# Performance work log

Hardware: AMD Instinct MI355X
Metric: run time of the kernel (lower is better)

Reference implementation:

```python
import jax, jax.numpy as jnp
import numpy as np

EPS_BN = 1e-5
DIVERSITY_TEMP = 100.0  # lucidrains codebook_diversity_temperature default
COMMIT_W = 1.0
DIVERSITY_W = 1.0
ORTHO_W = 1.0


def conv1d(x, w, b=None, stride=1, pad=0):
    # x: [B,C,T], w: [O,I,K] (torch layout)
    y = jax.lax.conv_general_dilated(x, w, (stride,), [(pad, pad)],
                                     dimension_numbers=('NCH', 'OIH', 'NCH'))
    if b is not None:
        y = y + b[None, :, None]
    return y


def conv1d_transpose(x, w_torch, stride, pad):
    # torch ConvTranspose1d weight: (in, out, k). Equivalent input-dilated conv
    # with flipped kernel and padding k-1-pad.
    w = jnp.flip(jnp.transpose(w_torch, (1, 0, 2)), axis=2)  # -> (out,in,k)
    k = w.shape[2]
    p = k - 1 - pad
    return jax.lax.conv_general_dilated(x, w, (1,), [(p, p)],
                                        lhs_dilation=(stride,),
                                        dimension_numbers=('NCH', 'OIH', 'NCH'))


def batchnorm(x, g, b):
    # training-mode BatchNorm1d: stats over (batch, time) per channel
    m = x.mean(axis=(0, 2), keepdims=True)
    v = x.var(axis=(0, 2), keepdims=True)
    return (x - m) * jax.lax.rsqrt(v + EPS_BN) * g[None, :, None] + b[None, :, None]


def setup_inputs():
    key = jax.random.key(0)
    ks = jax.random.split(key, 10)
    f32 = jnp.float32
    rn = lambda k, shape, s: jax.random.normal(k, shape, f32) * s
    return {
        'x': jax.random.normal(ks[0], (8, 1, 24000), f32),
        # encoder: 1->16->32->64
        'w1': rn(ks[1], (16, 1, 5), 0.3), 'b1': jnp.zeros(16, f32),
        'g1': jnp.ones(16, f32), 'be1': jnp.zeros(16, f32),
        'w2': rn(ks[2], (32, 16, 5), 0.1), 'b2': jnp.zeros(32, f32),
        'g2': jnp.ones(32, f32), 'be2': jnp.zeros(32, f32),
        'w3': rn(ks[3], (64, 32, 25), 0.05), 'b3': jnp.zeros(64, f32),
        'g3': jnp.ones(64, f32), 'be3': jnp.zeros(64, f32),
        # VQ codebook [codebook_size=8192, dim=64]
        'embed': jax.random.normal(ks[4], (8192, 64), f32),
        # decoder
        'dw1': rn(ks[5], (64, 64, 25), 0.05),  # ConvTranspose1d weight (in,out,k)
        'dg1': jnp.ones(64, f32), 'dbe1': jnp.zeros(64, f32),
        'dw2': rn(ks[6], (64, 64, 5), 0.1), 'db2': jnp.zeros(64, f32),
        'dg2': jnp.ones(64, f32), 'dbe2': jnp.zeros(64, f32),
        'dw3': rn(ks[7], (1, 64, 1), 0.2), 'db3': jnp.zeros(1, f32),
        # fixed random subset for orthogonal reg (orthogonal_reg_max_codes=256)
        'ortho_idx': jax.random.randint(ks[8], (256,), 0, 8192),
    }


def reference(x, w1, b1, g1, be1, w2, b2, g2, be2, w3, b3, g3, be3,
              embed, dw1, dg1, dbe1, dw2, db2, dg2, dbe2, dw3, db3, ortho_idx):
    # ---- encoder ----
    h = batchnorm(jax.nn.silu(conv1d(x, w1, b1, 1, 2)), g1, be1)
    h = batchnorm(jax.nn.silu(conv1d(h, w2, b2, 1, 2)), g2, be2)
    z = batchnorm(jnp.tanh(conv1d(h, w3, b3, 12, 12)), g3, be3)  # [B,64,N]
    B, C, N = z.shape
    zf = jnp.transpose(z, (0, 2, 1)).reshape(B * N, C)  # [B*N, 64]

    # ---- VQ: nearest neighbor over codebook ----
    d2 = (jnp.sum(zf * zf, -1, keepdims=True) - 2.0 * (zf @ embed.T)
          + jnp.sum(embed * embed, -1)[None, :])          # [B*N, K]
    dist = jnp.sqrt(jnp.clip(d2, 1e-12))                  # euclidean (cdist p=2)
    idx = jnp.argmin(d2, axis=-1)                         # [B*N]
    q = embed[idx]                                        # codebook gather

    commit = jnp.mean((jax.lax.stop_gradient(q) - zf) ** 2)

    prob = jax.nn.softmax(-dist * DIVERSITY_TEMP, axis=-1)
    avg_prob = prob.mean(axis=0)                          # [K]
    diversity = jnp.sum(avg_prob * jnp.log(jnp.clip(avg_prob, 1e-30)))

    codes = embed[ortho_idx]                              # [256, 64]
    normed = codes * jax.lax.rsqrt(jnp.sum(codes * codes, -1, keepdims=True) + 1e-12)
    cos = normed @ normed.T
    n = codes.shape[0]
    ortho = jnp.sum(cos * cos) / (n * n) - 1.0 / n

    loss = COMMIT_W * commit + DIVERSITY_W * diversity + ORTHO_W * ortho

    # straight-through estimator
    q_st = zf + jax.lax.stop_gradient(q - zf)
    zq = jnp.transpose(q_st.reshape(B, N, C), (0, 2, 1))  # [B,64,N]

    # ---- decoder ----
    d = batchnorm(jax.nn.silu(conv1d_transpose(zq, dw1, 12, 12)), dg1, dbe1)
    d = batchnorm(jax.nn.silu(conv1d(d, dw2, db2, 1, 2)), dg2, dbe2)
    recon = conv1d(d, dw3, db3, 1, 0)

    T = x.shape[2]
    cur = recon.shape[2]
    if cur > T:
        recon = recon[:, :, :T]
    elif cur < T:
        recon = jnp.pad(recon, ((0, 0), (0, 0), (0, T - cur)))
    return recon, idx.reshape(B, N), loss, (commit, diversity, ortho)
```

## Files before the change

kernel.cpp:

```cpp
#include <hip/hip_runtime.h>
#include <math.h>
#include <float.h>

#define DEV __device__ __forceinline__

#define BB 8
#define TT 24000
#define TD 23989
#define NZ 2000
#define ROWS 16000
#define NE 8192
#define NCG 8

typedef __attribute__((ext_vector_type(8))) short bf16x8;
typedef __attribute__((ext_vector_type(4))) float f32x4;

__device__ double g_st[640];
__device__ double g_misc[2];
__device__ float  g_e2[NE];
__device__ float  g_avg[NE];
__device__ float  g_z2[ROWS];
__device__ float  g_rdm[ROWS];
__device__ int    g_rix[ROWS];
__device__ float  g_ob[256 * 64];
__device__ float  g_pmd[ROWS * NCG];
__device__ int    g_pmi[ROWS * NCG];
__device__ int    g_pcc[ROWS * NCG];
__device__ float2 g_cand[ROWS * 256];
__device__ unsigned short g_zbh[ROWS * 64], g_zbl[ROWS * 64];
__device__ unsigned short g_ebh[NE * 64],  g_ebl[NE * 64];
__device__ float  g_s1[16], g_sh1[16];
__device__ float  g_s2[32], g_sh2[32];
__device__ float  g_sd1[64], g_shd1[64];
__device__ float  g_w2f[2560];
__device__ float  g_b2f[32];
__device__ float  g_w3f[64 * 32 * 25];
__device__ float  g_b3f[64];
__device__ float  g_dw2f[64 * 5 * 64];
__device__ float  g_db2f[64];
__device__ float  g_dw1t[64 * 64 * 25];
__device__ float  g_zbn[ROWS * 64];
__device__ double g_zbnd[ROWS * 64];
__device__ float  g_zq[BB * 64 * NZ];
__device__ float  g_y1[BB * 16 * TT];
__device__ float  g_zpre[BB * 64 * NZ];
__device__ float  g_yd1[BB * 64 * TD];
__device__ float  g_y2[BB * 32 * TT];
__device__ float  g_yd2[BB * 64 * TD];

DEV float wsum(float v){
  #pragma unroll
  for (int o = 32; o; o >>= 1) v += __shfl_xor(v, o, 64);
  return v;
}
DEV int clampc(int c){ return c < 0 ? 0 : (c > NE - 1 ? NE - 1 : c); }
DEV float bss(unsigned short s){ union { unsigned u; float f; } v; v.u = ((unsigned)s) << 16; return v.f; }
DEV unsigned short f2bs(float f){
  union { float f; unsigned u; } v; v.f = f;
  unsigned r = (v.u + 0x7FFF + ((v.u >> 16) & 1)) >> 16;
  return (unsigned short)r;
}

__global__ void k_zero(){
  int i = blockIdx.x * 256 + threadIdx.x;
  if (i < 640) g_st[i] = 0.0;
  if (i < 2) g_misc[i] = 0.0;
  if (i < NE) g_avg[i] = 0.f;
}

__global__ void k_embprep(const float* __restrict__ embed){
  int gt = blockIdx.x * 256 + threadIdx.x;
  int gs = gridDim.x * 256;
  for (int i = gt; i < NE * 64; i += gs){
    float v = embed[i];
    unsigned short h = f2bs(v);
    g_ebh[i] = h;
    g_ebl[i] = f2bs(v - bss(h));
  }
  for (int c = gt; c < NE; c += gs){
    float s = 0.f;
    for (int j = 0; j < 64; j++){ float v = embed[c * 64 + j]; s += v * v; }
    g_e2[c] = s;
  }
}

__global__ void k_zsplit(){
  int i = blockIdx.x * 256 + threadIdx.x;
  if (i < ROWS * 64){
    float v = g_zbn[i];
    unsigned short h = f2bs(v);
    g_zbh[i] = h;
    g_zbl[i] = f2bs(v - bss(h));
  }
}

__global__ void k_conv1(const float* __restrict__ x, const float* __restrict__ w1,
                        const float* __restrict__ b1){
  int b = blockIdx.y, t0 = blockIdx.x * 256, tid = threadIdx.x;
  __shared__ float xs[260], wl[80], bl[16], sacc[16], qacc[16];
  if (tid < 80) wl[tid] = w1[tid];
  if (tid < 16){ bl[tid] = b1[tid]; sacc[tid] = 0.f; qacc[tid] = 0.f; }
  for (int i = tid; i < 260; i += 256){ int g = t0 - 2 + i; xs[i] = ((unsigned)g < TT) ? x[b * TT + g] : 0.f; }
  __syncthreads();
  int t = t0 + tid;
  bool ok = t < TT;
  float xv[5];
  #pragma unroll
  for (int k = 0; k < 5; k++) xv[k] = xs[tid + k];
  float out[16];
  #pragma unroll
  for (int c = 0; c < 16; c++){
    float a = bl[c];
    #pragma unroll
    for (int k = 0; k < 5; k++) a += wl[c * 5 + k] * xv[k];
    float o = ok ? a / (1.f + expf(-a)) : 0.f;
    out[c] = o;
    if (ok) g_y1[(b * 16 + c) * TT + t] = o;
  }
  int lane = tid & 63;
  #pragma unroll
  for (int c = 0; c < 16; c++){
    float s = wsum(out[c]);
    float q = wsum(out[c] * out[c]);
    if (lane == 0){ atomicAdd(&sacc[c], s); atomicAdd(&qacc[c], q); }
  }
  __syncthreads();
  if (tid < 16){ atomicAdd(&g_st[tid * 2], (double)sacc[tid]); atomicAdd(&g_st[tid * 2 + 1], (double)qacc[tid]); }
}

__global__ void k_fold2(const float* __restrict__ g1, const float* __restrict__ be1,
                        const float* __restrict__ w2, const float* __restrict__ b2){
  int tid = threadIdx.x;
  if (blockIdx.x == 0 && tid < 16){
    double m = g_st[tid * 2] / 192000.0, v = g_st[tid * 2 + 1] / 192000.0 - m * m;
    float s = g1[tid] / sqrtf((float)v + 1e-5f);
    g_s1[tid] = s; g_sh1[tid] = be1[tid] - (float)m * s;
  }
  if (blockIdx.x == 0 && tid < 32) g_b2f[tid] = b2[tid];
  int gt = blockIdx.x * 256 + tid;
  for (int i = gt; i < 2560; i += 8 * 256){
    int co = i & 31, r = i >> 5, k = r % 5, ci = r / 5;
    g_w2f[i] = w2[(co * 16 + ci) * 5 + k];
  }
}

__global__ void __launch_bounds__(256) k_conv2(){
  int b = blockIdx.y, t0 = blockIdx.x * 256, tid = threadIdx.x;
  __shared__ float xs[16][260];
  __shared__ float sacc[32], qacc[32];
  __shared__ float s1l[16], sh1l[16];
  int lane = tid & 63, wv = tid >> 6;
  int cb = wv * 8;
  if (tid < 32){ sacc[tid] = 0.f; qacc[tid] = 0.f; }
  if (tid < 16){ s1l[tid] = g_s1[tid]; sh1l[tid] = g_sh1[tid]; }
  __syncthreads();
  for (int i = tid; i < 16 * 260; i += 256){
    int ci = i / 260, tt = i - ci * 260, g = t0 - 2 + tt;
    xs[ci][tt] = ((unsigned)g < TT) ? (s1l[ci] * g_y1[(b * 16 + ci) * TT + g] + sh1l[ci]) : 0.f;
  }
  __syncthreads();
  float acc[4][8];
  #pragma unroll
  for (int j = 0; j < 4; j++)
    #pragma unroll
    for (int i = 0; i < 8; i++) acc[j][i] = g_b2f[cb + i];
  for (int ci = 0; ci < 16; ci++){
    #pragma unroll
    for (int k = 0; k < 5; k++){
      const float4* wp = (const float4*)(g_w2f + (ci * 5 + k) * 32 + cb);
      float4 w0 = wp[0], w1v = wp[1];
      float wr[8] = { w0.x, w0.y, w0.z, w0.w, w1v.x, w1v.y, w1v.z, w1v.w };
      #pragma unroll
      for (int j = 0; j < 4; j++){
        float xv = xs[ci][lane + 64 * j + k];
        #pragma unroll
        for (int i = 0; i < 8; i++) acc[j][i] += wr[i] * xv;
      }
    }
  }
  #pragma unroll
  for (int i = 0; i < 8; i++){
    int co = cb + i;
    float s = 0.f, q = 0.f;
    #pragma unroll
    for (int j = 0; j < 4; j++){
      int t = t0 + lane + 64 * j;
      bool ok = t < TT;
      float a = acc[j][i];
      float o = ok ? a / (1.f + expf(-a)) : 0.f;
      if (ok) g_y2[(b * 32 + co) * TT + t] = o;
      s += o; q += o * o;
    }
    s = wsum(s); q = wsum(q);
    if (lane == 0){ atomicAdd(&sacc[co], s); atomicAdd(&qacc[co], q); }
  }
  __syncthreads();
  if (tid < 32){ atomicAdd(&g_st[128 + tid * 2], (double)sacc[tid]); atomicAdd(&g_st[128 + tid * 2 + 1], (double)qacc[tid]); }
}

__global__ void k_fold3(const float* __restrict__ g2, const float* __restrict__ be2,
                        const float* __restrict__ w3, const float* __restrict__ b3){
  int tid = threadIdx.x;
  if (blockIdx.x == 0 && tid < 32){
    double m = g_st[128 + tid * 2] / 192000.0, v = g_st[128 + tid * 2 + 1] / 192000.0 - m * m;
    float s = g2[tid] / sqrtf((float)v + 1e-5f);
    g_s2[tid] = s; g_sh2[tid] = be2[tid] - (float)m * s;
  }
  if (blockIdx.x == 0 && tid >= 64 && tid < 128) g_b3f[tid - 64] = b3[tid - 64];
  int gt = blockIdx.x * 256 + tid;
  for (int i = gt; i < 64 * 32 * 25; i += 64 * 256){
    int co = i & 63, r = i >> 6, k = r % 25, ci = r / 25;
    g_w3f[i] = w3[(co * 32 + ci) * 25 + k];
  }
}

__global__ void __launch_bounds__(256) k_conv3(){
  __shared__ float xs[32][400];
  __shared__ float s2l[32], sh2l[32];
  int tid = threadIdx.x, b = blockIdx.y, t0 = blockIdx.x * 32;
  int lane = tid & 63, wv = tid >> 6;
  int cb = wv * 16;
  int tl = lane & 31, h = lane >> 5;
  if (tid < 32){ s2l[tid] = g_s2[tid]; sh2l[tid] = g_sh2[tid]; }
  __syncthreads();
  int p0 = t0 * 12 - 12;
  for (int i = tid; i < 32 * 397; i += 256){
    int ci = i / 397, pp = i - ci * 397, g = p0 + pp;
    xs[ci][pp] = ((unsigned)g < TT) ? (s2l[ci] * g_y2[(b * 32 + ci) * TT + g] + sh2l[ci]) : 0.f;
  }
  __syncthreads();
  float acc[16];
  #pragma unroll
  for (int i = 0; i < 16; i++) acc[i] = 0.f;
  for (int cii = 0; cii < 16; cii++){
    int ci = h * 16 + cii;
    #pragma unroll
    for (int k = 0; k < 25; k++){
      float xv = xs[ci][tl * 12 + k];
      const float4* wp = (const float4*)(g_w3f + (ci * 25 + k) * 64 + cb);
      float4 a0 = wp[0], a1 = wp[1], a2 = wp[2], a3 = wp[3];
      acc[0] += a0.x * xv; acc[1] += a0.y * xv; acc[2] += a0.z * xv; acc[3] += a0.w * xv;
      acc[4] += a1.x * xv; acc[5] += a1.y * xv; acc[6] += a1.z * xv; acc[7] += a1.w * xv;
      acc[8] += a2.x * xv; acc[9] += a2.y * xv; acc[10] += a2.z * xv; acc[11] += a2.w * xv;
      acc[12] += a3.x * xv; acc[13] += a3.y * xv; acc[14] += a3.z * xv; acc[15] += a3.w * xv;
    }
  }
  #pragma unroll
  for (int i = 0; i < 16; i++) acc[i] += __shfl_xor(acc[i], 32, 64);
  int t = t0 + tl;
  if (h == 0 && t < NZ){
    #pragma unroll
    for (int i = 0; i < 16; i++)
      g_zpre[(b * 64 + cb + i) * NZ + t] = tanhf(acc[i] + g_b3f[cb + i]);
  }
}

__global__ void k_stats(int which, int L, int stoff){
  const float* p = (which == 0) ? g_zpre : (which == 1) ? g_yd1 : g_yd2;
  int co = blockIdx.y, t0 = blockIdx.x * 256, tid = threadIdx.x;
  int t = t0 + tid;
  float s = 0.f, q = 0.f;
  if (t < L){
    for (int b = 0; b < BB; b++){ float v = p[(b * 64 + co) * L + t]; s += v; q += v * v; }
  }
  s = wsum(s); q = wsum(q);
  __shared__ float sa[4], qa[4];
  int w = tid >> 6, lane = tid & 63;
  if (lane == 0){ sa[w] = s; qa[w] = q; }
  __syncthreads();
  if (tid == 0){
    atomicAdd(&g_st[stoff + co * 2], (double)(sa[0] + sa[1] + sa[2] + sa[3]));
    atomicAdd(&g_st[stoff + co * 2 + 1], (double)(qa[0] + qa[1] + qa[2] + qa[3]));
  }
}

__global__ void k_zbn(const float* __restrict__ g3, const float* __restrict__ be3){
  __shared__ float tile[64][65];
  __shared__ float s3[64], sh3[64];
  __shared__ double s3d[64], sh3d[64];
  int tid = threadIdx.x, b = blockIdx.y, n0 = blockIdx.x * 64;
  if (tid < 64){
    double m = g_st[256 + tid * 2] / 16000.0, v = g_st[256 + tid * 2 + 1] / 16000.0 - m * m;
    double sd = (double)g3[tid] / sqrt(v + 1e-5);
    double shd = (double)be3[tid] - m * sd;
    s3d[tid] = sd; sh3d[tid] = shd;
    s3[tid] = (float)sd; sh3[tid] = (float)shd;
  }
  __syncthreads();
  for (int i = tid; i < 64 * 64; i += 256){
    int c = i >> 6, nn = i & 63, n = n0 + nn;
    tile[c][nn] = (n < NZ) ? (s3[c] * g_zpre[(b * 64 + c) * NZ + n] + sh3[c]) : 0.f;
  }
  __syncthreads();
  int lane = tid & 63;
  for (int it = 0; it < 16; ++it){
    int nn = (tid >> 6) + it * 4;
    int n = n0 + nn, c = lane;
    if (n < NZ){
      float v = tile[c][nn];
      int row = b * NZ + n;
      g_zbn[row * 64 + c] = v;
      g_zbnd[row * 64 + c] = s3d[c] * (double)g_zpre[(b * 64 + c) * NZ + n] + sh3d[c];
      float s = wsum(v * v);
      if (lane == 0) g_z2[row] = s;
    }
  }
}

__global__ void __launch_bounds__(256) k_vq1(){
  __shared__ unsigned short bsh[64 * 72];
  __shared__ unsigned short bsl[64 * 72];
  __shared__ float2 ring[64][16];
  __shared__ int cnt[64];
  int tid = threadIdx.x, lane = tid & 63, w = tid >> 6;
  int q = lane >> 4, col = lane & 15;
  int rowbase = blockIdx.x * 64 + w * 16;
  int cbase = blockIdx.y * 1024;
  int grp = blockIdx.y;
  if (tid < 64) cnt[tid] = 0;
  #pragma unroll
  for (int i = 0; i < 4; i++)
    ring[w * 16 + (lane & 15)][(lane >> 4) * 4 + i] = make_float2(FLT_MAX, __int_as_float(NE - 1));
  bf16x8 ah0, ah1, al0, al1;
  {
    const unsigned short* zh = g_zbh + (rowbase + col) * 64;
    const unsigned short* zl = g_zbl + (rowbase + col) * 64;
    ah0 = *(const bf16x8*)(zh + q * 8);
    ah1 = *(const bf16x8*)(zh + 32 + q * 8);
    al0 = *(const bf16x8*)(zl + q * 8);
    al1 = *(const bf16x8*)(zl + 32 + q * 8);
  }
  float z2r[4];
  #pragma unroll
  for (int r = 0; r < 4; r++) z2r[r] = g_z2[rowbase + q * 4 + r];
  float thr[4], lmin[4]; int lamc[4];
  #pragma unroll
  for (int r = 0; r < 4; r++){ thr[r] = FLT_MAX; lmin[r] = FLT_MAX; lamc[r] = NE - 1; }
  float runmin[4] = {FLT_MAX, FLT_MAX, FLT_MAX, FLT_MAX};
  for (int ch = 0; ch < 16; ++ch){
    __syncthreads();
    {
      int cl = tid >> 2, seg = tid & 3;
      int cglob = cbase + ch * 64 + cl;
      *(int4*)&bsh[cl * 72 + seg * 16]     = *(const int4*)(g_ebh + cglob * 64 + seg * 16);
      *(int4*)&bsh[cl * 72 + seg * 16 + 8] = *(const int4*)(g_ebh + cglob * 64 + seg * 16 + 8);
      *(int4*)&bsl[cl * 72 + seg * 16]     = *(const int4*)(g_ebl + cglob * 64 + seg * 16);
      *(int4*)&bsl[cl * 72 + seg * 16 + 8] = *(const int4*)(g_ebl + cglob * 64 + seg * 16 + 8);
    }
    __syncthreads();
    float d2s[4][4];
    float tmin[4] = {FLT_MAX, FLT_MAX, FLT_MAX, FLT_MAX};
    #pragma unroll
    for (int t = 0; t < 4; t++){
      int ct = cbase + ch * 64 + t * 16;
      const unsigned short* bhp = &bsh[(t * 16 + col) * 72];
      const unsigned short* blp = &bsl[(t * 16 + col) * 72];
      bf16x8 bh0 = *(const bf16x8*)(bhp + q * 8);
      bf16x8 bh1 = *(const bf16x8*)(bhp + 32 + q * 8);
      bf16x8 bl0 = *(const bf16x8*)(blp + q * 8);
      bf16x8 bl1 = *(const bf16x8*)(blp + 32 + q * 8);
      f32x4 acc = {0.f, 0.f, 0.f, 0.f};
      acc = __builtin_amdgcn_mfma_f32_16x16x32_bf16(al0, bh0, acc, 0, 0, 0);
      acc = __builtin_amdgcn_mfma_f32_16x16x32_bf16(al1, bh1, acc, 0, 0, 0);
      acc = __builtin_amdgcn_mfma_f32_16x16x32_bf16(ah0, bl0, acc, 0, 0, 0);
      acc = __builtin_amdgcn_mfma_f32_16x16x32_bf16(ah1, bl1, acc, 0, 0, 0);
      acc = __builtin_amdgcn_mfma_f32_16x16x32_bf16(ah0, bh0, acc, 0, 0, 0);
      acc = __builtin_amdgcn_mfma_f32_16x16x32_bf16(ah1, bh1, acc, 0, 0, 0);
      float e2c = g_e2[ct + col];
      #pragma unroll
      for (int r = 0; r < 4; r++){
        float d = z2r[r] + e2c - 2.f * acc[r];
        d2s[t][r] = d;
        if (d < lmin[r]){ lmin[r] = d; lamc[r] = ct + col; }
        tmin[r] = fminf(tmin[r], d);
      }
    }
    #pragma unroll
    for (int r = 0; r < 4; r++){
      float m = tmin[r];
      m = fminf(m, __shfl_xor(m, 1, 64));
      m = fminf(m, __shfl_xor(m, 2, 64));
      m = fminf(m, __shfl_xor(m, 4, 64));
      m = fminf(m, __shfl_xor(m, 8, 64));
      if (m < runmin[r]){
        runmin[r] = m;
        thr[r] = m + 0.71f * sqrtf(fmaxf(m, 0.f)) + 0.13f;
      }
    }
    #pragma unroll
    for (int t = 0; t < 4; t++){
      int ct = cbase + ch * 64 + t * 16;
      bool any = false;
      #pragma unroll
      for (int r = 0; r < 4; r++) if (d2s[t][r] < thr[r]) any = true;
      if (__ballot(any)){
        #pragma unroll
        for (int r = 0; r < 4; r++){
          if (d2s[t][r] < thr[r]){
            int lr = w * 16 + q * 4 + r;
            int s = atomicAdd(&cnt[lr], 1) & 15;
            ring[lr][s] = make_float2(sqrtf(fmaxf(d2s[t][r], 1e-12f)), __int_as_float(ct + col));
          }
        }
      }
    }
  }
  __syncthreads();
  #pragma unroll
  for (int r = 0; r < 4; r++){
    float m = lmin[r]; int c = lamc[r];
    #pragma unroll
    for (int o = 1; o <= 8; o <<= 1){
      float om = __shfl_xor(m, o, 64);
      int oc = __shfl_xor(c, o, 64);
      if (om < m || (om == m && oc < c)){ m = om; c = oc; }
    }
    if (col == 0){
      int gr = rowbase + q * 4 + r;
      g_pmd[gr * NCG + grp] = m;
      g_pmi[gr * NCG + grp] = c;
    }
  }
  if (lane < 16){
    int lr = w * 16 + lane;
    g_pcc[(rowbase + lane) * NCG + grp] = cnt[lr];
  }
  #pragma unroll
  for (int i = 0; i < 4; i++){
    int idx = lane * 4 + i;
    int lr = idx >> 4, s = idx & 15;
    g_cand[(rowbase + lr) * 256 + grp * 16 + s] = ring[w * 16 + lr][s];
  }
}

__global__ void k_vq1b(){
  int row = blockIdx.x * 256 + threadIdx.x;
  if (row >= ROWS) return;
  float best = FLT_MAX; int bi = NE - 1;
  for (int cg = 0; cg < NCG; ++cg){
    float d = g_pmd[row * NCG + cg]; int i = g_pmi[row * NCG + cg];
    if (d < best || (d == best && i < bi)){ best = d; bi = i; }
  }
  g_rdm[row] = sqrtf(fmaxf(best, 1e-12f));
  g_rix[row] = bi;
}

__global__ void __launch_bounds__(256) k_vq3(const float* __restrict__ embed,
                                             float* __restrict__ outIdx){
  __shared__ int   ccode[4][144];
  __shared__ float cdst[4][144];
  __shared__ int   cn[4];
  __shared__ double bsum[4];
  int w = threadIdx.x >> 6, lane = threadIdx.x & 63;
  int row = blockIdx.x * 4 + w;
  float dmin = g_rdm[row];
  int seedc = clampc(g_rix[row]);
  if (lane == 0){ cn[w] = 0; ccode[w][0] = seedc; }
  __syncthreads();
  if (lane == 0) cn[w] = 1;
  int grp = lane & 7;
  int sub = lane >> 3;
  int cnt = g_pcc[row * NCG + grp]; if (cnt > 16) cnt = 16;
  int s0 = sub * 2, s1 = s0 + 2; if (s1 > cnt) s1 = cnt;
  for (int s = s0; s < s1; ++s){
    float2 cd = g_cand[row * 256 + grp * 16 + s];
    float dist = cd.x; int c = clampc(__float_as_int(cd.y));
    if (dist <= dmin + 0.353f && c != seedc){
      int i = atomicAdd(&cn[w], 1);
      ccode[w][i] = c;
    }
  }
  __syncthreads();
  int n = cn[w];
  double zdl = g_zbnd[row * 64 + lane];
  double bd = DBL_MAX; int bc = NE - 1;
  for (int i = 0; i < n; i++){
    int c = ccode[w][i];
    double diff = zdl - (double)embed[c * 64 + lane];
    double d = diff * diff;
    #pragma unroll
    for (int o = 32; o; o >>= 1) d += __shfl_xor(d, o, 64);
    if (lane == 0) cdst[w][i] = (float)d;
    if (d < bd || (d == bd && c < bc)){ bd = d; bc = c; }
  }
  __syncthreads();
  float dminE = (float)sqrt(bd);
  float Zp = 0.f;
  for (int i = lane; i < n; i += 64)
    Zp += expf(-100.f * (sqrtf(cdst[w][i]) - dminE));
  float Z = fmaxf(wsum(Zp), 1e-30f);
  if (lane == 0){
    g_rix[row] = bc;
    outIdx[row] = (float)bc;
    bsum[w] = bd;
  }
  for (int i = lane; i < n; i += 64)
    atomicAdd(&g_avg[ccode[w][i]], expf(-100.f * (sqrtf(cdst[w][i]) - dminE)) / Z);
  __syncthreads();
  if (threadIdx.x == 0)
    atomicAdd(&g_misc[0], bsum[0] + bsum[1] + bsum[2] + bsum[3]);
}

__global__ void k_orthoprep(const float* __restrict__ embed, const int* __restrict__ oidx){
  int tid = threadIdx.x;
  int c = clampc(oidx[tid]);
  float s = 0.f;
  for (int j = 0; j < 64; j++){ float v = embed[c * 64 + j]; s += v * v; }
  float r = 1.f / sqrtf(s + 1e-12f);
  for (int j = 0; j < 64; j++) g_ob[tid * 64 + j] = embed[c * 64 + j] * r;
}

__global__ void k_ortho(){
  int w = threadIdx.x >> 6, lane = threadIdx.x & 63;
  int i = blockIdx.x * 4 + w;
  float acc = 0.f;
  for (int j = lane; j < 256; j += 64){
    float d = 0.f;
    for (int k = 0; k < 64; k++) d += g_ob[i * 64 + k] * g_ob[j * 64 + k];
    acc += d * d;
  }
  acc = wsum(acc);
  if (lane == 0) atomicAdd(&g_misc[1], (double)acc);
}

__global__ void k_div(float* __restrict__ outS){
  int tid = threadIdx.x;
  double part = 0.0;
  for (int c = tid; c < NE; c += 256){
    double p = (double)g_avg[c] / 16000.0;
    double pc = p < 1e-30 ? 1e-30 : p;
    part += p * log(pc);
  }
  __shared__ double red[256];
  red[tid] = part; __syncthreads();
  for (int o = 128; o; o >>= 1){ if (tid < o) red[tid] += red[tid + o]; __syncthreads(); }
  if (tid == 0){
    double diversity = red[0];
    double commit = g_misc[0] / (double)(ROWS * 64);
    double ortho = g_misc[1] / 65536.0 - 1.0 / 256.0;
    double loss = commit + diversity + ortho;
    outS[0] = (float)loss;
    outS[1] = (float)commit;
    outS[2] = (float)diversity;
    outS[3] = (float)ortho;
  }
}

__global__ void k_zq(const float* __restrict__ embed){
  __shared__ float tile[64][65];
  int tid = threadIdx.x, b = blockIdx.y, n0 = blockIdx.x * 64;
  for (int i = tid; i < 64 * 64; i += 256){
    int nn = i >> 6, c = i & 63;
    int n = n0 + nn;
    int code = (n < NZ) ? clampc(g_rix[b * NZ + n]) : 0;
    tile[c][nn] = embed[code * 64 + c];
  }
  __syncthreads();
  for (int i = tid; i < 64 * 64; i += 256){
    int c = i >> 6, nn = i & 63;
    int n = n0 + nn;
    if (n < NZ) g_zq[(b * 64 + c) * NZ + n] = tile[c][nn];
  }
}

__global__ void k_folddw1(const float* __restrict__ dw1){
  int gt = blockIdx.x * 256 + threadIdx.x;
  for (int i = gt; i < 64 * 64 * 25; i += 100 * 256){
    int co = i & 63, r = i >> 6, k = r % 25, ci = r / 25;
    g_dw1t[i] = dw1[(ci * 64 + co) * 25 + (24 - k)];
  }
}

__global__ void __launch_bounds__(256, 3) k_dconv1(){
  __shared__ float xsd[16][260];
  __shared__ float wsh[4][64][28];
  __shared__ float sacc[4], qacc[4];
  int tid = threadIdx.x, b = blockIdx.y;
  int cb = blockIdx.z * 4;
  int t0 = blockIdx.x * 3072;
  int nb = blockIdx.x * 256 - 1;
  int w = tid >> 6, lane = tid & 63;
  if (tid < 4){ sacc[tid] = 0.f; qacc[tid] = 0.f; }
  for (int i = tid; i < 6400; i += 256){
    int c = i & 3, r = i >> 2;
    int k = r % 25, ci = r / 25;
    wsh[c][ci][k] = g_dw1t[r * 64 + cb + c];
  }
  float acc[4][12];
  #pragma unroll
  for (int q = 0; q < 4; q++)
    #pragma unroll
    for (int p = 0; p < 12; p++) acc[q][p] = 0.f;
  for (int cc = 0; cc < 4; ++cc){
    __syncthreads();
    for (int i = tid; i < 16 * 259; i += 256){
      int ci = i / 259, nl = i - ci * 259;
      int n = nb + nl;
      xsd[ci][nl] = ((unsigned)n < NZ) ? g_zq[(b * 64 + cc * 16 + ci) * NZ + n] : 0.f;
    }
    __syncthreads();
    #pragma unroll 2
    for (int ci = 0; ci < 16; ++ci){
      int cia = cc * 16 + ci;
      const float4* xp = (const float4*)&xsd[ci][4 * lane];
      float4 xA = xp[0], xB = xp[1];
      float xv[6] = { xA.x, xA.y, xA.z, xA.w, xB.x, xB.y };
      const float4* wp = (const float4*)&wsh[w][cia][0];
      float4 w0 = wp[0], w1 = wp[1], w2 = wp[2], w3 = wp[3], w4 = wp[4], w5 = wp[5];
      float wv[25] = { w0.x, w0.y, w0.z, w0.w, w1.x, w1.y, w1.z, w1.w,
                       w2.x, w2.y, w2.z, w2.w, w3.x, w3.y, w3.z, w3.w,
                       w4.x, w4.y, w4.z, w4.w, w5.x, w5.y, w5.z, w5.w,
                       wsh[w][cia][24] };
      #pragma unroll
      for (int q = 0; q < 4; ++q){
        acc[q][0] += wv[0] * xv[q];
        acc[q][0] += wv[12] * xv[q + 1];
        acc[q][0] += wv[24] * xv[q + 2];
        #pragma unroll
        for (int p = 1; p < 12; ++p){
          acc[q][p] += wv[12 - p] * xv[q + 1];
          acc[q][p] += wv[24 - p] * xv[q + 2];
        }
      }
    }
  }
  bool full = (t0 + 3072 <= TD);
  float s = 0.f, qs = 0.f;
  float* dst = &g_yd1[(b * 64 + cb + w) * TD + t0 + lane * 48];
  #pragma unroll
  for (int q = 0; q < 4; ++q){
    float o[12];
    #pragma unroll
    for (int p = 0; p < 12; ++p){
      int t = t0 + lane * 48 + q * 12 + p;
      float a = acc[q][p];
      float v = (t < TD) ? a / (1.f + expf(-a)) : 0.f;
      o[p] = v; s += v; qs += v * v;
    }
    if (full){
      ((float4*)(dst + q * 12))[0] = make_float4(o[0], o[1], o[2], o[3]);
      ((float4*)(dst + q * 12))[1] = make_float4(o[4], o[5], o[6], o[7]);
      ((float4*)(dst + q * 12))[2] = make_float4(o[8], o[9], o[10], o[11]);
    } else {
      #pragma unroll
      for (int p = 0; p < 12; ++p){
        int t = t0 + lane * 48 + q * 12 + p;
        if (t < TD) dst[q * 12 + p] = o[p];
      }
    }
  }
  s = wsum(s); qs = wsum(qs);
  if (lane == 0){ atomicAdd(&sacc[w], s); atomicAdd(&qacc[w], qs); }
  __syncthreads();
  if (tid < 4){
    atomicAdd(&g_st[384 + (cb + tid) * 2], (double)sacc[tid]);
    atomicAdd(&g_st[384 + (cb + tid) * 2 + 1], (double)qacc[tid]);
  }
}

__global__ void k_foldd2(const float* __restrict__ dg1, const float* __restrict__ dbe1,
                         const float* __restrict__ dw2, const float* __restrict__ db2){
  int tid = threadIdx.x;
  if (blockIdx.x == 0 && tid < 64){
    double m = g_st[384 + tid * 2] / 191912.0, v = g_st[384 + tid * 2 + 1] / 191912.0 - m * m;
    float sc = dg1[tid] / sqrtf((float)v + 1e-5f);
    g_sd1[tid] = sc; g_shd1[tid] = dbe1[tid] - (float)m * sc;
    g_db2f[tid] = db2[tid];
  }
  int gt = blockIdx.x * 256 + tid;
  for (int i = gt; i < 64 * 5 * 64; i += 32 * 256){
    int co = i & 63, r = i >> 6, k = r % 5, ci = r / 5;
    g_dw2f[i] = dw2[(co * 64 + ci) * 5 + k];
  }
}

__global__ void __launch_bounds__(256) k_dconv2(){
  __shared__ float xs[32][132];
  __shared__ float sdl[64], shdl[64];
  __shared__ float sacc[64], qacc[64];
  int tid = threadIdx.x, b = blockIdx.y, t0 = blockIdx.x * 128;
  int lane = tid & 63, wv = tid >> 6;
  int cb = wv * 16;
  if (tid < 64){ sdl[tid] = g_sd1[tid]; shdl[tid] = g_shd1[tid]; sacc[tid] = 0.f; qacc[tid] = 0.f; }
  float acc[2][16];
  #pragma unroll
  for (int j = 0; j < 2; j++)
    #pragma unroll
    for (int i = 0; i < 16; i++) acc[j][i] = g_db2f[cb + i];
  for (int half = 0; half < 2; ++half){
    __syncthreads();
    for (int i = tid; i < 32 * 132; i += 256){
      int ci = i / 132, tt = i - ci * 132, g = t0 - 2 + tt;
      int cia = half * 32 + ci;
      xs[ci][tt] = ((unsigned)g < TD) ? (sdl[cia] * g_yd1[(b * 64 + cia) * TD + g] + shdl[cia]) : 0.f;
    }
    __syncthreads();
    for (int ci = 0; ci < 32; ci++){
      int cia = half * 32 + ci;
      #pragma unroll
      for (int k = 0; k < 5; k++){
        const float4* wp = (const float4*)(g_dw2f + (cia * 5 + k) * 64 + cb);
        float4 w0 = wp[0], w1 = wp[1], w2v = wp[2], w3v = wp[3];
        float wr[16] = { w0.x, w0.y, w0.z, w0.w, w1.x, w1.y, w1.z, w1.w,
                         w2v.x, w2v.y, w2v.z, w2v.w, w3v.x, w3v.y, w3v.z, w3v.w };
        #pragma unroll
        for (int j = 0; j < 2; j++){
          float xv = xs[ci][lane + 64 * j + k];
          #pragma unroll
          for (int i = 0; i < 16; i++) acc[j][i] += wr[i] * xv;
        }
      }
    }
  }
  #pragma unroll
  for (int i = 0; i < 16; i++){
    int co = cb + i;
    float s = 0.f, q = 0.f;
    #pragma unroll
    for (int j = 0; j < 2; j++){
      int t = t0 + lane + 64 * j;
      bool ok = t < TD;
      float a = acc[j][i];
      float o = ok ? a / (1.f + expf(-a)) : 0.f;
      if (ok) g_yd2[(b * 64 + co) * TD + t] = o;
      s += o; q += o * o;
    }
    s = wsum(s); q = wsum(q);
    if (lane == 0){ atomicAdd(&sacc[co], s); atomicAdd(&qacc[co], q); }
  }
  __syncthreads();
  if (tid < 64){
    atomicAdd(&g_st[512 + tid * 2], (double)sacc[tid]);
    atomicAdd(&g_st[512 + tid * 2 + 1], (double)qacc[tid]);
  }
}

__global__ void k_recon(const float* __restrict__ dg2, const float* __restrict__ dbe2,
                        const float* __restrict__ dw3, const float* __restrict__ db3,
                        float* __restrict__ outR){
  __shared__ float wf[64];
  __shared__ float bsh2;
  int tid = threadIdx.x, b = blockIdx.y, t0 = blockIdx.x * 256;
  if (tid < 64){
    double m = g_st[512 + tid * 2] / 191912.0, v = g_st[512 + tid * 2 + 1] / 191912.0 - m * m;
    float sc = dg2[tid] / sqrtf((float)v + 1e-5f);
    float shv = dbe2[tid] - (float)m * sc;
    wf[tid] = dw3[tid] * sc;
    float contrib = wsum(dw3[tid] * shv);
    if (tid == 0) bsh2 = db3[0] + contrib;
  }
  __syncthreads();
  int t = t0 + tid;
  if (t < TT){
    if (t < TD){
      float a = bsh2;
      for (int ci = 0; ci < 64; ci++) a += wf[ci] * g_yd2[(b * 64 + ci) * TD + t];
      outR[b * TT + t] = a;
    } else {
      outR[b * TT + t] = 0.f;
    }
  }
}

extern "C" void kernel_launch(void* const* d_in, const int* in_sizes, int n_in,
                              void* d_out, int out_size, void* d_ws, size_t ws_size,
                              hipStream_t stream){
  (void)in_sizes; (void)n_in; (void)out_size; (void)d_ws; (void)ws_size;
  const float* x    = (const float*)d_in[0];
  const float* w1   = (const float*)d_in[1];
  const float* b1   = (const float*)d_in[2];
  const float* g1   = (const float*)d_in[3];
  const float* be1  = (const float*)d_in[4];
  const float* w2   = (const float*)d_in[5];
  const float* b2   = (const float*)d_in[6];
  const float* g2   = (const float*)d_in[7];
  const float* be2  = (const float*)d_in[8];
  const float* w3   = (const float*)d_in[9];
  const float* b3   = (const float*)d_in[10];
  const float* g3   = (const float*)d_in[11];
  const float* be3  = (const float*)d_in[12];
  const float* embed= (const float*)d_in[13];
  const float* dw1  = (const float*)d_in[14];
  const float* dg1  = (const float*)d_in[15];
  const float* dbe1 = (const float*)d_in[16];
  const float* dw2  = (const float*)d_in[17];
  const float* db2  = (const float*)d_in[18];
  const float* dg2  = (const float*)d_in[19];
  const float* dbe2 = (const float*)d_in[20];
  const float* dw3  = (const float*)d_in[21];
  const float* db3  = (const float*)d_in[22];
  const int* oidx   = (const int*)d_in[23];

  float* out    = (float*)d_out;
  float* outIdx = out + 192000;
  float* outS   = out + 208000;

  hipLaunchKernelGGL(k_zero, dim3(32), dim3(256), 0, stream);
  hipLaunchKernelGGL(k_embprep, dim3(64), dim3(256), 0, stream, embed);
  hipLaunchKernelGGL(k_conv1, dim3(94, 8), dim3(256), 0, stream, x, w1, b1);
  hipLaunchKernelGGL(k_fold2, dim3(8), dim3(256), 0, stream, g1, be1, w2, b2);
  hipLaunchKernelGGL(k_conv2, dim3(94, 8), dim3(256), 0, stream);
  hipLaunchKernelGGL(k_fold3, dim3(64), dim3(256), 0, stream, g2, be2, w3, b3);
  hipLaunchKernelGGL(k_conv3, dim3(63, 8), dim3(256), 0, stream);
  hipLaunchKernelGGL(k_stats, dim3(8, 64), dim3(256), 0, stream, 0, NZ, 256);
  hipLaunchKernelGGL(k_zbn, dim3(32, 8), dim3(256), 0, stream, g3, be3);
  hipLaunchKernelGGL(k_zsplit, dim3(4000), dim3(256), 0, stream);
  hipLaunchKernelGGL(k_vq1, dim3(250, 8), dim3(256), 0, stream);
  hipLaunchKernelGGL(k_vq1b, dim3(63), dim3(256), 0, stream);
  hipLaunchKernelGGL(k_vq3, dim3(4000), dim3(256), 0, stream, embed, outIdx);
  hipLaunchKernelGGL(k_orthoprep, dim3(1), dim3(256), 0, stream, embed, oidx);
  hipLaunchKernelGGL(k_ortho, dim3(64), dim3(256), 0, stream);
  hipLaunchKernelGGL(k_div, dim3(1), dim3(256), 0, stream, outS);
  hipLaunchKernelGGL(k_zq, dim3(32, 8), dim3(256), 0, stream, embed);
  hipLaunchKernelGGL(k_folddw1, dim3(100), dim3(256), 0, stream, dw1);
  hipLaunchKernelGGL(k_dconv1, dim3(8, 8, 16), dim3(256), 0, stream);
  hipLaunchKernelGGL(k_foldd2, dim3(32), dim3(256), 0, stream, dg1, dbe1, dw2, db2);
  hipLaunchKernelGGL(k_dconv2, dim3(188, 8), dim3(256), 0, stream);
  hipLaunchKernelGGL(k_recon, dim3(94, 8), dim3(256), 0, stream, dg2, dbe2, dw3, db3, out);
}
```

Baseline: 963.4 us.

## Retile decoder conv2 with register blocking, shared-memory weights and vector stores

```diff
diff --git a/kernel.cpp b/kernel.cpp
--- a/kernel.cpp
+++ b/kernel.cpp
@@ -674,64 +674,94 @@
   }
 }
 
-__global__ void __launch_bounds__(256) k_dconv2(){
-  __shared__ float xs[32][132];
+__global__ void __launch_bounds__(256, 2) k_dconv2(){
+  __shared__ float xs[16][772];
+  __shared__ float wch[16 * 5 * 32];
   __shared__ float sdl[64], shdl[64];
-  __shared__ float sacc[64], qacc[64];
-  int tid = threadIdx.x, b = blockIdx.y, t0 = blockIdx.x * 128;
+  __shared__ float sacc[32], qacc[32];
+  int tid = threadIdx.x, b = blockIdx.y, bz = blockIdx.z;
+  int t0 = blockIdx.x * 768;
   int lane = tid & 63, wv = tid >> 6;
-  int cb = wv * 16;
-  if (tid < 64){ sdl[tid] = g_sd1[tid]; shdl[tid] = g_shd1[tid]; sacc[tid] = 0.f; qacc[tid] = 0.f; }
-  float acc[2][16];
-  #pragma unroll
-  for (int j = 0; j < 2; j++)
-    #pragma unroll
-    for (int i = 0; i < 16; i++) acc[j][i] = g_db2f[cb + i];
-  for (int half = 0; half < 2; ++half){
+  int cb = bz * 32 + wv * 8;
+  if (tid < 64){ sdl[tid] = g_sd1[tid]; shdl[tid] = g_shd1[tid]; }
+  if (tid < 32){ sacc[tid] = 0.f; qacc[tid] = 0.f; }
+  float acc[12][8];
+  #pragma unroll
+  for (int j = 0; j < 12; j++)
+    #pragma unroll
+    for (int i = 0; i < 8; i++) acc[j][i] = g_db2f[cb + i];
+  for (int ch = 0; ch < 4; ++ch){
     __syncthreads();
-    for (int i = tid; i < 32 * 132; i += 256){
-      int ci = i / 132, tt = i - ci * 132, g = t0 - 2 + tt;
-      int cia = half * 32 + ci;
+    for (int i = tid; i < 16 * 772; i += 256){
+      int ci = i / 772, tt = i - ci * 772, g = t0 - 2 + tt;
+      int cia = ch * 16 + ci;
       xs[ci][tt] = ((unsigned)g < TD) ? (sdl[cia] * g_yd1[(b * 64 + cia) * TD + g] + shdl[cia]) : 0.f;
     }
+    for (int i = tid; i < 2560; i += 256){
+      int r = i >> 5, c = i & 31;
+      wch[i] = g_dw2f[(ch * 80 + r) * 64 + bz * 32 + c];
+    }
     __syncthreads();
-    for (int ci = 0; ci < 32; ci++){
-      int cia = half * 32 + ci;
+    for (int ci = 0; ci < 16; ++ci){
+      float xv[3][8];
       #pragma unroll
-      for (int k = 0; k < 5; k++){
-        const float4* wp = (const float4*)(g_dw2f + (cia * 5 + k) * 64 + cb);
-        float4 w0 = wp[0], w1 = wp[1], w2v = wp[2], w3v = wp[3];
-        float wr[16] = { w0.x, w0.y, w0.z, w0.w, w1.x, w1.y, w1.z, w1.w,
-                         w2v.x, w2v.y, w2v.z, w2v.w, w3v.x, w3v.y, w3v.z, w3v.w };
+      for (int j4 = 0; j4 < 3; ++j4){
+        const float4* xp = (const float4*)&xs[ci][j4 * 256 + 4 * lane];
+        float4 a = xp[0], bq = xp[1];
+        xv[j4][0] = a.x;  xv[j4][1] = a.y;  xv[j4][2] = a.z;  xv[j4][3] = a.w;
+        xv[j4][4] = bq.x; xv[j4][5] = bq.y; xv[j4][6] = bq.z; xv[j4][7] = bq.w;
+      }
+      #pragma unroll
+      for (int k = 0; k < 5; ++k){
+        const float4* wp = (const float4*)(wch + (ci * 5 + k) * 32 + wv * 8);
+        float4 w0 = wp[0], w1 = wp[1];
+        float wr[8] = { w0.x, w0.y, w0.z, w0.w, w1.x, w1.y, w1.z, w1.w };
         #pragma unroll
-        for (int j = 0; j < 2; j++){
-          float xv = xs[ci][lane + 64 * j + k];
+        for (int j4 = 0; j4 < 3; ++j4){
           #pragma unroll
-          for (int i = 0; i < 16; i++) acc[j][i] += wr[i] * xv;
+          for (int jj = 0; jj < 4; ++jj){
+            float xvv = xv[j4][jj + k];
+            #pragma unroll
+            for (int i = 0; i < 8; i++) acc[j4 * 4 + jj][i] += wr[i] * xvv;
+          }
         }
       }
     }
   }
-  #pragma unroll
-  for (int i = 0; i < 16; i++){
+  bool full = (t0 + 768 <= TD);
+  #pragma unroll
+  for (int i = 0; i < 8; i++){
     int co = cb + i;
     float s = 0.f, q = 0.f;
-    #pragma unroll
-    for (int j = 0; j < 2; j++){
-      int t = t0 + lane + 64 * j;
-      bool ok = t < TD;
-      float a = acc[j][i];
-      float o = ok ? a / (1.f + expf(-a)) : 0.f;
-      if (ok) g_yd2[(b * 64 + co) * TD + t] = o;
-      s += o; q += o * o;
+    float* dst = &g_yd2[(b * 64 + co) * TD + t0 + lane * 4];
+    #pragma unroll
+    for (int j4 = 0; j4 < 3; ++j4){
+      float o[4];
+      #pragma unroll
+      for (int jj = 0; jj < 4; ++jj){
+        int t = t0 + j4 * 256 + lane * 4 + jj;
+        float a = acc[j4 * 4 + jj][i];
+        float v = (t < TD) ? a / (1.f + expf(-a)) : 0.f;
+        o[jj] = v; s += v; q += v * v;
+      }
+      if (full){
+        *(float4*)(dst + j4 * 256) = make_float4(o[0], o[1], o[2], o[3]);
+      } else {
+        #pragma unroll
+        for (int jj = 0; jj < 4; ++jj){
+          int t = t0 + j4 * 256 + lane * 4 + jj;
+          if (t < TD) dst[j4 * 256 + jj] = o[jj];
+        }
+      }
     }
     s = wsum(s); q = wsum(q);
-    if (lane == 0){ atomicAdd(&sacc[co], s); atomicAdd(&qacc[co], q); }
-  }
-  __syncthreads();
-  if (tid < 64){
-    atomicAdd(&g_st[512 + tid * 2], (double)sacc[tid]);
-    atomicAdd(&g_st[512 + tid * 2 + 1], (double)qacc[tid]);
+    if (lane == 0){ atomicAdd(&sacc[wv * 8 + i], s); atomicAdd(&qacc[wv * 8 + i], q); }
+  }
+  __syncthreads();
+  if (tid < 32){
+    int co = bz * 32 + tid;
+    atomicAdd(&g_st[512 + co * 2], (double)sacc[tid]);
+    atomicAdd(&g_st[512 + co * 2 + 1], (double)qacc[tid]);
   }
 }
 
@@ -815,6 +845,6 @@
   hipLaunchKernelGGL(k_folddw1, dim3(100), dim3(256), 0, stream, dw1);
   hipLaunchKernelGGL(k_dconv1, dim3(8, 8, 16), dim3(256), 0, stream);
   hipLaunchKernelGGL(k_foldd2, dim3(32), dim3(256), 0, stream, dg1, dbe1, dw2, db2);
-  hipLaunchKernelGGL(k_dconv2, dim3(188, 8), dim3(256), 0, stream);
+  hipLaunchKernelGGL(k_dconv2, dim3(32, 8, 2), dim3(256), 0, stream);
   hipLaunchKernelGGL(k_recon, dim3(94, 8), dim3(256), 0, stream, dg2, dbe2, dw3, db3, out);
 }
```

New measurement: 862.2 us. 10.5% less time.

## Rewrite decoder conv2 as split-bf16 MFMA with swizzled LDS tiles

Applied to the files above, without the earlier changes.

```diff
diff --git a/kernel.cpp b/kernel.cpp
--- a/kernel.cpp
+++ b/kernel.cpp
@@ -36,7 +36,8 @@
 __device__ float  g_b2f[32];
 __device__ float  g_w3f[64 * 32 * 25];
 __device__ float  g_b3f[64];
-__device__ float  g_dw2f[64 * 5 * 64];
+__device__ unsigned short g_dwh[5 * 2 * 64 * 32];
+__device__ unsigned short g_dwl[5 * 2 * 64 * 32];
 __device__ float  g_db2f[64];
 __device__ float  g_dw1t[64 * 64 * 25];
 __device__ float  g_zbn[ROWS * 64];
@@ -668,65 +669,102 @@
     g_db2f[tid] = db2[tid];
   }
   int gt = blockIdx.x * 256 + tid;
-  for (int i = gt; i < 64 * 5 * 64; i += 32 * 256){
-    int co = i & 63, r = i >> 6, k = r % 5, ci = r / 5;
-    g_dw2f[i] = dw2[(co * 64 + ci) * 5 + k];
-  }
-}
-
-__global__ void __launch_bounds__(256) k_dconv2(){
-  __shared__ float xs[32][132];
-  __shared__ float sdl[64], shdl[64];
+  for (int i = gt; i < 20480; i += 32 * 256){
+    int ciL = i & 31;
+    int r = i >> 5;
+    int co = r & 63;
+    int r2 = r >> 6;
+    int c = r2 & 1, k = r2 >> 1;
+    float w = dw2[(co * 64 + c * 32 + ciL) * 5 + k];
+    unsigned short h = f2bs(w);
+    g_dwh[i] = h;
+    g_dwl[i] = f2bs(w - bss(h));
+  }
+}
+
+__global__ void __launch_bounds__(256, 2) k_dconv2(){
+  __shared__ unsigned short xh[36 * 64];
+  __shared__ unsigned short xl[36 * 64];
   __shared__ float sacc[64], qacc[64];
-  int tid = threadIdx.x, b = blockIdx.y, t0 = blockIdx.x * 128;
+  int tid = threadIdx.x, b = blockIdx.y;
+  int t0 = blockIdx.x * 32;
   int lane = tid & 63, wv = tid >> 6;
-  int cb = wv * 16;
-  if (tid < 64){ sdl[tid] = g_sd1[tid]; shdl[tid] = g_shd1[tid]; sacc[tid] = 0.f; qacc[tid] = 0.f; }
-  float acc[2][16];
-  #pragma unroll
-  for (int j = 0; j < 2; j++)
-    #pragma unroll
-    for (int i = 0; i < 16; i++) acc[j][i] = g_db2f[cb + i];
-  for (int half = 0; half < 2; ++half){
-    __syncthreads();
-    for (int i = tid; i < 32 * 132; i += 256){
-      int ci = i / 132, tt = i - ci * 132, g = t0 - 2 + tt;
-      int cia = half * 32 + ci;
-      xs[ci][tt] = ((unsigned)g < TD) ? (sdl[cia] * g_yd1[(b * 64 + cia) * TD + g] + shdl[cia]) : 0.f;
-    }
-    __syncthreads();
-    for (int ci = 0; ci < 32; ci++){
-      int cia = half * 32 + ci;
-      #pragma unroll
-      for (int k = 0; k < 5; k++){
-        const float4* wp = (const float4*)(g_dw2f + (cia * 5 + k) * 64 + cb);
-        float4 w0 = wp[0], w1 = wp[1], w2v = wp[2], w3v = wp[3];
-        float wr[16] = { w0.x, w0.y, w0.z, w0.w, w1.x, w1.y, w1.z, w1.w,
-                         w2v.x, w2v.y, w2v.z, w2v.w, w3v.x, w3v.y, w3v.z, w3v.w };
-        #pragma unroll
-        for (int j = 0; j < 2; j++){
-          float xv = xs[ci][lane + 64 * j + k];
-          #pragma unroll
-          for (int i = 0; i < 16; i++) acc[j][i] += wr[i] * xv;
-        }
-      }
-    }
-  }
-  #pragma unroll
-  for (int i = 0; i < 16; i++){
-    int co = cb + i;
-    float s = 0.f, q = 0.f;
-    #pragma unroll
-    for (int j = 0; j < 2; j++){
-      int t = t0 + lane + 64 * j;
-      bool ok = t < TD;
-      float a = acc[j][i];
-      float o = ok ? a / (1.f + expf(-a)) : 0.f;
-      if (ok) g_yd2[(b * 64 + co) * TD + t] = o;
-      s += o; q += o * o;
-    }
-    s = wsum(s); q = wsum(q);
-    if (lane == 0){ atomicAdd(&sacc[co], s); atomicAdd(&qacc[co], q); }
+  int q = lane >> 4, tcol = lane & 15;
+  int cobase = wv * 16;
+  if (tid < 64){ sacc[tid] = 0.f; qacc[tid] = 0.f; }
+
+  bf16x8 wh[10], wl[10];
+  {
+    int co = cobase + tcol;
+    #pragma unroll
+    for (int kc = 0; kc < 10; ++kc){
+      wh[kc] = *(const bf16x8*)(g_dwh + (kc * 64 + co) * 32 + q * 8);
+      wl[kc] = *(const bf16x8*)(g_dwl + (kc * 64 + co) * 32 + q * 8);
+    }
+  }
+
+  for (int it = 0; it < 16; ++it){
+    int ci = wv * 16 + it;
+    if (lane < 36){
+      int g = t0 - 2 + lane;
+      float sdv = g_sd1[ci], shv = g_shd1[ci];
+      float val = ((unsigned)g < TD) ? (sdv * g_yd1[(size_t)(b * 64 + ci) * TD + g] + shv) : 0.f;
+      unsigned short h = f2bs(val);
+      unsigned short lo = f2bs(val - bss(h));
+      int off = lane * 128 + ((ci * 2) ^ ((lane & 7) << 4));
+      *(unsigned short*)((char*)xh + off) = h;
+      *(unsigned short*)((char*)xl + off) = lo;
+    }
+  }
+  __syncthreads();
+
+  f32x4 acc0, acc1;
+  #pragma unroll
+  for (int r = 0; r < 4; ++r){
+    float bsv = g_db2f[cobase + q * 4 + r];
+    acc0[r] = bsv; acc1[r] = bsv;
+  }
+  #pragma unroll
+  for (int k = 0; k < 5; ++k){
+    #pragma unroll
+    for (int c = 0; c < 2; ++c){
+      int kc = k * 2 + c;
+      int gl0 = k + tcol;
+      int off0 = gl0 * 128 + ((c * 64 + q * 16) ^ ((gl0 & 7) << 4));
+      bf16x8 x0h = *(const bf16x8*)((const char*)xh + off0);
+      bf16x8 x0l = *(const bf16x8*)((const char*)xl + off0);
+      acc0 = __builtin_amdgcn_mfma_f32_16x16x32_bf16(wh[kc], x0l, acc0, 0, 0, 0);
+      acc0 = __builtin_amdgcn_mfma_f32_16x16x32_bf16(wl[kc], x0h, acc0, 0, 0, 0);
+      acc0 = __builtin_amdgcn_mfma_f32_16x16x32_bf16(wh[kc], x0h, acc0, 0, 0, 0);
+      int gl1 = gl0 + 16;
+      int off1 = gl1 * 128 + ((c * 64 + q * 16) ^ ((gl1 & 7) << 4));
+      bf16x8 x1h = *(const bf16x8*)((const char*)xh + off1);
+      bf16x8 x1l = *(const bf16x8*)((const char*)xl + off1);
+      acc1 = __builtin_amdgcn_mfma_f32_16x16x32_bf16(wh[kc], x1l, acc1, 0, 0, 0);
+      acc1 = __builtin_amdgcn_mfma_f32_16x16x32_bf16(wl[kc], x1h, acc1, 0, 0, 0);
+      acc1 = __builtin_amdgcn_mfma_f32_16x16x32_bf16(wh[kc], x1h, acc1, 0, 0, 0);
+    }
+  }
+
+  #pragma unroll
+  for (int r = 0; r < 4; ++r){
+    int co = cobase + q * 4 + r;
+    float* dst = &g_yd2[(size_t)(b * 64 + co) * TD];
+    int ta = t0 + tcol;
+    float a0 = acc0[r];
+    float o0 = (ta < TD) ? a0 / (1.f + expf(-a0)) : 0.f;
+    if (ta < TD) dst[ta] = o0;
+    int tb = ta + 16;
+    float a1 = acc1[r];
+    float o1 = (tb < TD) ? a1 / (1.f + expf(-a1)) : 0.f;
+    if (tb < TD) dst[tb] = o1;
+    float sv = o0 + o1, qv = o0 * o0 + o1 * o1;
+    #pragma unroll
+    for (int o = 1; o <= 8; o <<= 1){ sv += __shfl_xor(sv, o, 64); qv += __shfl_xor(qv, o, 64); }
+    if (tcol == 0){
+      atomicAdd(&sacc[co], sv);
+      atomicAdd(&qacc[co], qv);
+    }
   }
   __syncthreads();
   if (tid < 64){
@@ -815,6 +853,6 @@
   hipLaunchKernelGGL(k_folddw1, dim3(100), dim3(256), 0, stream, dw1);
   hipLaunchKernelGGL(k_dconv1, dim3(8, 8, 16), dim3(256), 0, stream);
   hipLaunchKernelGGL(k_foldd2, dim3(32), dim3(256), 0, stream, dg1, dbe1, dw2, db2);
-  hipLaunchKernelGGL(k_dconv2, dim3(188, 8), dim3(256), 0, stream);
+  hipLaunchKernelGGL(k_dconv2, dim3(750, 8), dim3(256), 0, stream);
   hipLaunchKernelGGL(k_recon, dim3(94, 8), dim3(256), 0, stream, dg2, dbe2, dw3, db3, out);
 }
```

Result: slower. 1.089 ms (+13.0%).
